# Kernel tuning notes

Measured on AMD Instinct MI355X. Metric: run time of the kernel, lower is better.

The kernel has to match this reference:

```python
import jax, jax.numpy as jnp
import numpy as np

N, TD, TE, D = 8, 1024, 2048, 1024

def setup_inputs() -> dict:
    key = jax.random.key(0)
    kq, km, kl = jax.random.split(key, 3)
    queries = jax.random.normal(kq, (N, TD, D), dtype=jnp.float32)
    memory = jax.random.normal(km, (N, TE, D), dtype=jnp.float32)
    # lengths in [1, TE] so no row is fully masked (avoids NaN softmax)
    lengths = jax.random.randint(kl, (N,), 1, TE + 1, dtype=jnp.int32)
    return {"queries": queries, "memory": memory, "lengths": lengths}

def reference(queries, memory, lengths):
    scale = jnp.asarray(np.sqrt(D), dtype=queries.dtype)
    # [N, Td, Te] = bmm(queries, memory^T) / sqrt(D)
    weights = jnp.einsum('ntd,nsd->nts', queries, memory) / scale
    # padding mask: position s is invalid if s >= lengths[n]
    mask = jnp.arange(TE)[None, :] >= lengths[:, None]          # [N, Te]
    weights = jnp.where(mask[:, None, :], -jnp.inf, weights)
    alignments = jax.nn.softmax(weights, axis=-1)               # [N, Td, Te]
    contexts = jnp.einsum('nts,nsd->ntd', alignments, memory)   # [N, Td, D]
    return (contexts, alignments)
```

## Files before the change

kernel.cpp:

```cpp
#include <hip/hip_runtime.h>
#include <hip/hip_bf16.h>

#define NB 8
#define TDIM 1024
#define TEDIM 2048
#define DDIM 1024

typedef __bf16 bf16x8 __attribute__((ext_vector_type(8)));
typedef float f32x4 __attribute__((ext_vector_type(4)));
typedef unsigned short us8 __attribute__((ext_vector_type(8)));

static __device__ __forceinline__ void gld_lds16(const __bf16* g, __bf16* l) {
    __builtin_amdgcn_global_load_lds(
        (const __attribute__((address_space(1))) void*)g,
        (__attribute__((address_space(3))) void*)l,
        16, 0, 0);
}

static __device__ __forceinline__ unsigned short bf16_bits(float f) {
    __bf16 h = (__bf16)f;
    return __builtin_bit_cast(unsigned short, h);
}

__global__ __launch_bounds__(256) void cast_bf16_kernel(
    const float* __restrict__ src, __bf16* __restrict__ dst)
{
    const size_t i = ((size_t)blockIdx.x * 256 + threadIdx.x) * 8;
    float4 a = *reinterpret_cast<const float4*>(&src[i]);
    float4 b = *reinterpret_cast<const float4*>(&src[i + 4]);
    us8 o;
    o[0] = bf16_bits(a.x); o[1] = bf16_bits(a.y);
    o[2] = bf16_bits(a.z); o[3] = bf16_bits(a.w);
    o[4] = bf16_bits(b.x); o[5] = bf16_bits(b.y);
    o[6] = bf16_bits(b.z); o[7] = bf16_bits(b.w);
    *reinterpret_cast<us8*>(&dst[i]) = o;
}

__global__ __launch_bounds__(256) void transpose_cast_m_kernel(
    const float* __restrict__ M, __bf16* __restrict__ Mb,
    __bf16* __restrict__ Mt)
{
    const int n  = blockIdx.z;
    const int s0 = blockIdx.x * 64;
    const int d0 = blockIdx.y * 64;
    const float* Mn  = M  + (size_t)n * TEDIM * DDIM;
    __bf16*      Mbn = Mb + (size_t)n * TEDIM * DDIM;
    __bf16*      Mtn = Mt + (size_t)n * DDIM * TEDIM;

    __shared__ float tile[64][65];
    const int t = threadIdx.x;

    #pragma unroll
    for (int j = 0; j < 4; ++j) {
        const int flat = j * 256 + t;
        const int r  = flat >> 4;
        const int c4 = (flat & 15) * 4;
        float4 v = *reinterpret_cast<const float4*>(
            &Mn[(size_t)(s0 + r) * DDIM + d0 + c4]);
        tile[r][c4 + 0] = v.x; tile[r][c4 + 1] = v.y;
        tile[r][c4 + 2] = v.z; tile[r][c4 + 3] = v.w;
        ushort4 o;
        o.x = bf16_bits(v.x); o.y = bf16_bits(v.y);
        o.z = bf16_bits(v.z); o.w = bf16_bits(v.w);
        *reinterpret_cast<ushort4*>(&Mbn[(size_t)(s0 + r) * DDIM + d0 + c4]) = o;
    }
    __syncthreads();

    const int dr  = t >> 2;
    const int sc0 = (t & 3) * 16;
    us8 o0, o1;
    #pragma unroll
    for (int i = 0; i < 8; ++i)  o0[i] = bf16_bits(tile[sc0 + i][dr]);
    #pragma unroll
    for (int i = 0; i < 8; ++i)  o1[i] = bf16_bits(tile[sc0 + 8 + i][dr]);
    __bf16* dst = &Mtn[(size_t)(d0 + dr) * TEDIM + s0 + sc0];
    *reinterpret_cast<us8*>(dst)     = o0;
    *reinterpret_cast<us8*>(dst + 8) = o1;
}

template<int LDA, int LDB, int LDC, int KDIM, bool SCALE>
__global__ __launch_bounds__(256) void gemm_bt_kernel(
    const __bf16* __restrict__ A, const __bf16* __restrict__ B,
    float* __restrict__ C)
{
    const int n    = blockIdx.z;
    const int row0 = blockIdx.x * 128;
    const int col0 = blockIdx.y * 128;

    const __bf16* Ab = A + (size_t)n * gridDim.x * 128 * LDA + (size_t)row0 * LDA;
    const __bf16* Bb = B + (size_t)n * gridDim.y * 128 * LDB + (size_t)col0 * LDB;
    float*        Cb = C + (size_t)n * gridDim.x * 128 * LDC;

    __shared__ __align__(16) __bf16 As[128 * 32];
    __shared__ __align__(16) __bf16 Bs[128 * 32];

    const int t    = threadIdx.x;
    const int lane = t & 63;
    const int w    = t >> 6;
    const int wr   = (w >> 1) * 64;
    const int wc   = (w & 1) * 64;

    f32x4 acc[4][4] = {};

    for (int k0 = 0; k0 < KDIM; k0 += 32) {
        #pragma unroll
        for (int j = 0; j < 2; ++j) {
            const int tt = j * 256 + t;
            const int r  = tt >> 2;
            const int c  = (tt & 3) * 8;
            gld_lds16(Ab + (size_t)r * LDA + k0 + c, &As[tt * 8]);
            gld_lds16(Bb + (size_t)r * LDB + k0 + c, &Bs[tt * 8]);
        }
        __syncthreads();

        bf16x8 af[4], bfr[4];
        #pragma unroll
        for (int i = 0; i < 4; ++i)
            af[i] = *reinterpret_cast<const bf16x8*>(
                &As[(wr + i * 16 + (lane & 15)) * 32 + (lane >> 4) * 8]);
        #pragma unroll
        for (int j = 0; j < 4; ++j)
            bfr[j] = *reinterpret_cast<const bf16x8*>(
                &Bs[(wc + j * 16 + (lane & 15)) * 32 + (lane >> 4) * 8]);

        #pragma unroll
        for (int i = 0; i < 4; ++i)
            #pragma unroll
            for (int j = 0; j < 4; ++j)
                acc[i][j] = __builtin_amdgcn_mfma_f32_16x16x32_bf16(
                    af[i], bfr[j], acc[i][j], 0, 0, 0);
        __syncthreads();
    }

    const float sc = SCALE ? 0.03125f : 1.0f;
    #pragma unroll
    for (int i = 0; i < 4; ++i) {
        #pragma unroll
        for (int j = 0; j < 4; ++j) {
            const int col   = col0 + wc + j * 16 + (lane & 15);
            const int rbase = row0 + wr + i * 16 + (lane >> 4) * 4;
            #pragma unroll
            for (int r = 0; r < 4; ++r)
                Cb[(size_t)(rbase + r) * LDC + col] = acc[i][j][r] * sc;
        }
    }
}

__global__ __launch_bounds__(256) void softmax_kernel(
    float* __restrict__ S, __bf16* __restrict__ Pb,
    const int* __restrict__ len_p)
{
    const int row = blockIdx.x;
    const int n   = row >> 10;
    const int len = len_p[n];
    float*  Sr  = S  + (size_t)row * TEDIM;
    __bf16* Pr  = Pb + (size_t)row * TEDIM;

    const int t    = threadIdx.x;
    const int lane = t & 63;
    const int w    = t >> 6;
    const int s0   = t * 8;

    float4 a = *reinterpret_cast<const float4*>(&Sr[s0]);
    float4 b = *reinterpret_cast<const float4*>(&Sr[s0 + 4]);
    float v[8] = {a.x, a.y, a.z, a.w, b.x, b.y, b.z, b.w};
    #pragma unroll
    for (int i = 0; i < 8; ++i)
        if (s0 + i >= len) v[i] = -INFINITY;

    float mx = v[0];
    #pragma unroll
    for (int i = 1; i < 8; ++i) mx = fmaxf(mx, v[i]);
    #pragma unroll
    for (int off = 32; off; off >>= 1) mx = fmaxf(mx, __shfl_xor(mx, off));

    __shared__ float redm[4], reds[4];
    if (lane == 0) redm[w] = mx;
    __syncthreads();
    mx = fmaxf(fmaxf(redm[0], redm[1]), fmaxf(redm[2], redm[3]));

    float e[8];
    float sum = 0.f;
    #pragma unroll
    for (int i = 0; i < 8; ++i) { e[i] = __expf(v[i] - mx); sum += e[i]; }
    #pragma unroll
    for (int off = 32; off; off >>= 1) sum += __shfl_xor(sum, off);
    if (lane == 0) reds[w] = sum;
    __syncthreads();
    sum = reds[0] + reds[1] + reds[2] + reds[3];

    const float r = 1.0f / sum;
    float4 oa = {e[0] * r, e[1] * r, e[2] * r, e[3] * r};
    float4 ob = {e[4] * r, e[5] * r, e[6] * r, e[7] * r};
    *reinterpret_cast<float4*>(&Sr[s0])     = oa;
    *reinterpret_cast<float4*>(&Sr[s0 + 4]) = ob;

    us8 o;
    o[0] = bf16_bits(oa.x); o[1] = bf16_bits(oa.y);
    o[2] = bf16_bits(oa.z); o[3] = bf16_bits(oa.w);
    o[4] = bf16_bits(ob.x); o[5] = bf16_bits(ob.y);
    o[6] = bf16_bits(ob.z); o[7] = bf16_bits(ob.w);
    *reinterpret_cast<us8*>(&Pr[s0]) = o;
}

extern "C" void kernel_launch(void* const* d_in, const int* in_sizes, int n_in,
                              void* d_out, int out_size, void* d_ws, size_t ws_size,
                              hipStream_t stream) {
    const float* Q       = (const float*)d_in[0];
    const float* M       = (const float*)d_in[1];
    const int*   lengths = (const int*)d_in[2];

    float* ctx   = (float*)d_out;
    float* align = ctx + (size_t)NB * TDIM * DDIM;

    __bf16* Qb = (__bf16*)d_ws;
    __bf16* Mb = Qb + (size_t)NB * TDIM * DDIM;
    __bf16* Mt = Mb + (size_t)NB * TEDIM * DDIM;
    __bf16* Pb = Mt + (size_t)NB * DDIM * TEDIM;

    dim3 blk(256);
    cast_bf16_kernel<<<dim3(NB * TDIM * DDIM / (8 * 256)), blk, 0, stream>>>(Q, Qb);
    transpose_cast_m_kernel<<<dim3(TEDIM / 64, DDIM / 64, NB), blk, 0, stream>>>(M, Mb, Mt);
    gemm_bt_kernel<DDIM, DDIM, TEDIM, DDIM, true>
        <<<dim3(TDIM / 128, TEDIM / 128, NB), blk, 0, stream>>>(Qb, Mb, align);
    softmax_kernel<<<dim3(NB * TDIM), blk, 0, stream>>>(align, Pb, lengths);
    gemm_bt_kernel<TEDIM, TEDIM, DDIM, TEDIM, false>
        <<<dim3(TDIM / 128, DDIM / 128, NB), blk, 0, stream>>>(Pb, Mt, ctx);
}
```

Baseline: 320.1 us.

## Store scores as bf16 and remap GEMM blocks for batch-interleaved L2 locality

The first GEMM now writes its scaled scores as bf16 into the probability buffer instead of fp32 into the alignments output. Softmax reads those bf16 scores and writes the fp32 alignments plus the bf16 probabilities in place, which cuts score write and read traffic roughly in half. Both GEMMs also linearise the block index so batches interleave in the low bits and rows are grouped into tiles, aiming at better L2 reuse. Rounding the scores to bf16 before softmax costs logit precision, which could hurt accuracy on the alignments output.

```diff
diff --git a/kernel.cpp b/kernel.cpp
--- a/kernel.cpp
+++ b/kernel.cpp
@@ -20,6 +20,9 @@
 static __device__ __forceinline__ unsigned short bf16_bits(float f) {
     __bf16 h = (__bf16)f;
     return __builtin_bit_cast(unsigned short, h);
+}
+static __device__ __forceinline__ float bits_f32(unsigned short u) {
+    return (float)__builtin_bit_cast(__bf16, u);
 }
 
 __global__ __launch_bounds__(256) void cast_bf16_kernel(
@@ -78,18 +81,23 @@
     *reinterpret_cast<us8*>(dst + 8) = o1;
 }
 
-template<int LDA, int LDB, int LDC, int KDIM, bool SCALE>
+template<int LDA, int LDB, int LDC, int KDIM, int GX, int GY, int GR,
+         bool SCALE, bool OUTBF16>
 __global__ __launch_bounds__(256) void gemm_bt_kernel(
     const __bf16* __restrict__ A, const __bf16* __restrict__ B,
-    float* __restrict__ C)
-{
-    const int n    = blockIdx.z;
-    const int row0 = blockIdx.x * 128;
-    const int col0 = blockIdx.y * 128;
-
-    const __bf16* Ab = A + (size_t)n * gridDim.x * 128 * LDA + (size_t)row0 * LDA;
-    const __bf16* Bb = B + (size_t)n * gridDim.y * 128 * LDB + (size_t)col0 * LDB;
-    float*        Cb = C + (size_t)n * gridDim.x * 128 * LDC;
+    void* __restrict__ Cv)
+{
+    constexpr int PER_B = GX * GY;
+    const int L   = blockIdx.x + GX * (blockIdx.y + GY * blockIdx.z);
+    const int n   = L & 7;
+    const int rem = L >> 3;
+    const int rg  = rem / (GR * GY);
+    const int r2  = rem % (GR * GY);
+    const int row0 = (rg * GR + (r2 % GR)) * 128;
+    const int col0 = (r2 / GR) * 128;
+
+    const __bf16* Ab = A + (size_t)n * GX * 128 * LDA + (size_t)row0 * LDA;
+    const __bf16* Bb = B + (size_t)n * GY * 128 * LDB + (size_t)col0 * LDB;
 
     __shared__ __align__(16) __bf16 As[128 * 32];
     __shared__ __align__(16) __bf16 Bs[128 * 32];
@@ -140,33 +148,40 @@
             const int col   = col0 + wc + j * 16 + (lane & 15);
             const int rbase = row0 + wr + i * 16 + (lane >> 4) * 4;
             #pragma unroll
-            for (int r = 0; r < 4; ++r)
-                Cb[(size_t)(rbase + r) * LDC + col] = acc[i][j][r] * sc;
+            for (int r = 0; r < 4; ++r) {
+                const size_t idx =
+                    (size_t)n * GX * 128 * LDC + (size_t)(rbase + r) * LDC + col;
+                if constexpr (OUTBF16)
+                    ((__bf16*)Cv)[idx] = (__bf16)(acc[i][j][r] * sc);
+                else
+                    ((float*)Cv)[idx] = acc[i][j][r] * sc;
+            }
         }
     }
 }
 
 __global__ __launch_bounds__(256) void softmax_kernel(
-    float* __restrict__ S, __bf16* __restrict__ Pb,
+    __bf16* __restrict__ P, float* __restrict__ Sout,
     const int* __restrict__ len_p)
 {
     const int row = blockIdx.x;
     const int n   = row >> 10;
     const int len = len_p[n];
-    float*  Sr  = S  + (size_t)row * TEDIM;
-    __bf16* Pr  = Pb + (size_t)row * TEDIM;
+    __bf16* Pr = P    + (size_t)row * TEDIM;
+    float*  Sr = Sout + (size_t)row * TEDIM;
 
     const int t    = threadIdx.x;
     const int lane = t & 63;
     const int w    = t >> 6;
     const int s0   = t * 8;
 
-    float4 a = *reinterpret_cast<const float4*>(&Sr[s0]);
-    float4 b = *reinterpret_cast<const float4*>(&Sr[s0 + 4]);
-    float v[8] = {a.x, a.y, a.z, a.w, b.x, b.y, b.z, b.w};
-    #pragma unroll
-    for (int i = 0; i < 8; ++i)
+    us8 raw = *reinterpret_cast<const us8*>(&Pr[s0]);
+    float v[8];
+    #pragma unroll
+    for (int i = 0; i < 8; ++i) {
+        v[i] = bits_f32(raw[i]);
         if (s0 + i >= len) v[i] = -INFINITY;
+    }
 
     float mx = v[0];
     #pragma unroll
@@ -190,16 +205,18 @@
     sum = reds[0] + reds[1] + reds[2] + reds[3];
 
     const float r = 1.0f / sum;
-    float4 oa = {e[0] * r, e[1] * r, e[2] * r, e[3] * r};
-    float4 ob = {e[4] * r, e[5] * r, e[6] * r, e[7] * r};
+    float p[8];
+    #pragma unroll
+    for (int i = 0; i < 8; ++i) p[i] = e[i] * r;
+
+    float4 oa = {p[0], p[1], p[2], p[3]};
+    float4 ob = {p[4], p[5], p[6], p[7]};
     *reinterpret_cast<float4*>(&Sr[s0])     = oa;
     *reinterpret_cast<float4*>(&Sr[s0 + 4]) = ob;
 
     us8 o;
-    o[0] = bf16_bits(oa.x); o[1] = bf16_bits(oa.y);
-    o[2] = bf16_bits(oa.z); o[3] = bf16_bits(oa.w);
-    o[4] = bf16_bits(ob.x); o[5] = bf16_bits(ob.y);
-    o[6] = bf16_bits(ob.z); o[7] = bf16_bits(ob.w);
+    #pragma unroll
+    for (int i = 0; i < 8; ++i) o[i] = bf16_bits(p[i]);
     *reinterpret_cast<us8*>(&Pr[s0]) = o;
 }
 
@@ -221,9 +238,9 @@
     dim3 blk(256);
     cast_bf16_kernel<<<dim3(NB * TDIM * DDIM / (8 * 256)), blk, 0, stream>>>(Q, Qb);
     transpose_cast_m_kernel<<<dim3(TEDIM / 64, DDIM / 64, NB), blk, 0, stream>>>(M, Mb, Mt);
-    gemm_bt_kernel<DDIM, DDIM, TEDIM, DDIM, true>
-        <<<dim3(TDIM / 128, TEDIM / 128, NB), blk, 0, stream>>>(Qb, Mb, align);
-    softmax_kernel<<<dim3(NB * TDIM), blk, 0, stream>>>(align, Pb, lengths);
-    gemm_bt_kernel<TEDIM, TEDIM, DDIM, TEDIM, false>
-        <<<dim3(TDIM / 128, DDIM / 128, NB), blk, 0, stream>>>(Pb, Mt, ctx);
-}
+    gemm_bt_kernel<DDIM, DDIM, TEDIM, DDIM, 8, 16, 8, true, true>
+        <<<dim3(8, 16, NB), blk, 0, stream>>>(Qb, Mb, (void*)Pb);
+    softmax_kernel<<<dim3(NB * TDIM), blk, 0, stream>>>(Pb, align, lengths);
+    gemm_bt_kernel<TEDIM, TEDIM, DDIM, TEDIM, 8, 8, 4, false, false>
+        <<<dim3(8, 8, NB), blk, 0, stream>>>(Pb, Mt, (void*)ctx);
+}
```

Result: faster. 296.3 us (-7.5%).
